# Kernel optimization log

Hardware: AMD Instinct MI355X
Metric: run time of the kernel (lower is better)

Reference implementation:

```python
import jax, jax.numpy as jnp
import numpy as np

DIM = 64  # matches init kwarg `dim`


def setup_inputs() -> dict:
    key = jax.random.key(0)
    k1, k2, k3, k4 = jax.random.split(key, 4)
    B, S, D = 16, 4096, DIM
    query = jax.random.normal(k1, (B, S, D), dtype=jnp.float32)
    key_t = jax.random.normal(k2, (B, S, D), dtype=jnp.float32)
    value = jax.random.normal(k3, (B, S, D), dtype=jnp.float32)
    mask = jax.random.randint(k4, (B, S), 0, 2).astype(jnp.bool_)
    return {"query": query, "key": key_t, "value": value, "mask": mask}


def reference(query, key, value, mask):
    # score: [B, Sq, Sk]
    scale = 1.0 / np.sqrt(DIM).astype(np.float32)
    score = jnp.einsum("bqd,bkd->bqk", query, key) * scale
    # mask reshaped to [B, 1, Sk]; True positions filled with -inf
    score = jnp.where(mask[:, None, :], -jnp.inf, score)
    attn = jax.nn.softmax(score, axis=-1)
    # dropout_p = 0.0 -> identity
    context = jnp.einsum("bqk,bkd->bqd", attn, value)
    return (context, attn)
```

## Files before the change

kernel.cpp:

```cpp
#include <hip/hip_runtime.h>
#include <hip/hip_bf16.h>
#include <cstdint>
#include <cstddef>

#define B_   16
#define S_   4096
#define D_   64
#define TQ   64
#define TK   64
#define KSTR 72
#define VSTR 72
#define PSTR 72
#define CTX_ELEMS (B_*S_*D_)

typedef __attribute__((ext_vector_type(8))) short short8;
typedef __attribute__((ext_vector_type(4))) float f32x4;

static __device__ __forceinline__ unsigned short f2bf(float f) {
  union { float f; unsigned int u; } v; v.f = f;
  unsigned int r = (v.u + 0x7FFFu + ((v.u >> 16) & 1u)) >> 16;
  return (unsigned short)r;
}

__global__ __launch_bounds__(256) void conv_bf16_kernel(
    const float* __restrict__ src, unsigned short* __restrict__ dst) {
  int i = blockIdx.x * 256 + threadIdx.x;
  const float4* s = (const float4*)src;
  float4 a = s[(size_t)i*2], b = s[(size_t)i*2 + 1];
  unsigned int u0 = (unsigned)f2bf(a.x) | ((unsigned)f2bf(a.y) << 16);
  unsigned int u1 = (unsigned)f2bf(a.z) | ((unsigned)f2bf(a.w) << 16);
  unsigned int u2 = (unsigned)f2bf(b.x) | ((unsigned)f2bf(b.y) << 16);
  unsigned int u3 = (unsigned)f2bf(b.z) | ((unsigned)f2bf(b.w) << 16);
  uint4 o; o.x = u0; o.y = u1; o.z = u2; o.w = u3;
  *(uint4*)(dst + (size_t)i * 8) = o;
}

__global__ __launch_bounds__(256) void convVt_kernel(
    const float* __restrict__ V, unsigned short* __restrict__ Vt) {
  __shared__ unsigned short lsT[D_ * VSTR];
  const int tid = threadIdx.x;
  const int b = blockIdx.y, k0 = blockIdx.x * 64;
  const float4* src = (const float4*)(V + ((size_t)(b * S_ + k0)) * D_);
#pragma unroll
  for (int i = 0; i < 4; ++i) {
    int li = tid + 256 * i;
    int row = li >> 4, c4 = li & 15;
    float4 v = src[row * 16 + c4];
    lsT[(c4 * 4 + 0) * VSTR + row] = f2bf(v.x);
    lsT[(c4 * 4 + 1) * VSTR + row] = f2bf(v.y);
    lsT[(c4 * 4 + 2) * VSTR + row] = f2bf(v.z);
    lsT[(c4 * 4 + 3) * VSTR + row] = f2bf(v.w);
  }
  __syncthreads();
#pragma unroll
  for (int i = 0; i < 2; ++i) {
    int li = tid + 256 * i;
    int d = li >> 3, c = li & 7;
    uint4 v = *(const uint4*)&lsT[d * VSTR + c * 8];
    *(uint4*)(Vt + ((size_t)(b * D_ + d)) * S_ + k0 + c * 8) = v;
  }
}

template<bool PRE>
__global__ __launch_bounds__(256, 2) void attn_kernel(
    const float* __restrict__ Q,
    const unsigned short* __restrict__ K16,
    const unsigned short* __restrict__ Vt16,
    const float* __restrict__ K32,
    const float* __restrict__ V32,
    const int* __restrict__ mask,
    float* __restrict__ out) {
  __shared__ unsigned short lsK[TK * KSTR];
  __shared__ unsigned short lsV[D_ * VSTR];
  __shared__ unsigned short lsP[4 * 16 * PSTR];
  __shared__ float lsBias[S_];

  const int tid = threadIdx.x;
  const int wave = tid >> 6, lane = tid & 63;
  const int quad = lane >> 4, n = lane & 15;

  const int g = blockIdx.x;
  const int b = (g & 7) * 2 + ((g >> 3) & 1);
  const int qt = g >> 4;
  const int qbase = qt * TQ;
  const int bS = b * S_;

  for (int i = tid; i < S_; i += 256)
    lsBias[i] = mask[bS + i] ? -1e30f : 0.0f;

  const float QSC = 0.125f * 1.44269504088896340736f;
  const int qrowA = qbase + wave * 16 + n;
  const float* qp = Q + ((size_t)(bS + qrowA)) * D_ + quad * 8;
  short8 aq0, aq1;
  {
    float4 f0 = *(const float4*)(qp);
    float4 f1 = *(const float4*)(qp + 4);
    float4 f2 = *(const float4*)(qp + 32);
    float4 f3 = *(const float4*)(qp + 36);
    aq0[0] = (short)f2bf(f0.x * QSC); aq0[1] = (short)f2bf(f0.y * QSC);
    aq0[2] = (short)f2bf(f0.z * QSC); aq0[3] = (short)f2bf(f0.w * QSC);
    aq0[4] = (short)f2bf(f1.x * QSC); aq0[5] = (short)f2bf(f1.y * QSC);
    aq0[6] = (short)f2bf(f1.z * QSC); aq0[7] = (short)f2bf(f1.w * QSC);
    aq1[0] = (short)f2bf(f2.x * QSC); aq1[1] = (short)f2bf(f2.y * QSC);
    aq1[2] = (short)f2bf(f2.z * QSC); aq1[3] = (short)f2bf(f2.w * QSC);
    aq1[4] = (short)f2bf(f3.x * QSC); aq1[5] = (short)f2bf(f3.y * QSC);
    aq1[6] = (short)f2bf(f3.z * QSC); aq1[7] = (short)f2bf(f3.w * QSC);
  }

  float l0 = 0.f, l1 = 0.f, l2 = 0.f, l3 = 0.f;
  for (int kt = 0; kt < S_ / TK; ++kt) {
    const int k0 = kt * TK;
    __syncthreads();
    if (PRE) {
#pragma unroll
      for (int i = 0; i < 2; ++i) {
        int li = tid + 256 * i;
        int row = li >> 3, c = li & 7;
        uint4 v = *(const uint4*)(K16 + ((size_t)(bS + k0 + row)) * D_ + c * 8);
        *(uint4*)&lsK[row * KSTR + c * 8] = v;
      }
    } else {
#pragma unroll
      for (int i = 0; i < 4; ++i) {
        int li = tid + 256 * i;
        int row = li >> 4, c4 = li & 15;
        float4 v = *(const float4*)(K32 + ((size_t)(bS + k0 + row)) * D_ + c4 * 4);
        unsigned int u0 = (unsigned)f2bf(v.x) | ((unsigned)f2bf(v.y) << 16);
        unsigned int u1 = (unsigned)f2bf(v.z) | ((unsigned)f2bf(v.w) << 16);
        uint2 uu; uu.x = u0; uu.y = u1;
        *(uint2*)&lsK[row * KSTR + c4 * 4] = uu;
      }
    }
    __syncthreads();
#pragma unroll
    for (int ch = 0; ch < 4; ++ch) {
      short8 kb0 = *(const short8*)&lsK[(ch * 16 + n) * KSTR + quad * 8];
      short8 kb1 = *(const short8*)&lsK[(ch * 16 + n) * KSTR + 32 + quad * 8];
      f32x4 c = {0.f, 0.f, 0.f, 0.f};
      c = __builtin_amdgcn_mfma_f32_16x16x32_bf16(aq0, kb0, c, 0, 0, 0);
      c = __builtin_amdgcn_mfma_f32_16x16x32_bf16(aq1, kb1, c, 0, 0, 0);
      float bias = lsBias[k0 + ch * 16 + n];
      l0 += exp2f(c[0] + bias);
      l1 += exp2f(c[1] + bias);
      l2 += exp2f(c[2] + bias);
      l3 += exp2f(c[3] + bias);
    }
  }
  float rl[4];
  {
    float t[4] = {l0, l1, l2, l3};
#pragma unroll
    for (int r = 0; r < 4; ++r) {
      float x = t[r];
      x += __shfl_xor(x, 1); x += __shfl_xor(x, 2);
      x += __shfl_xor(x, 4); x += __shfl_xor(x, 8);
      rl[r] = 1.0f / x;
    }
  }

  f32x4 oc0 = {0.f,0.f,0.f,0.f}, oc1 = {0.f,0.f,0.f,0.f};
  f32x4 oc2 = {0.f,0.f,0.f,0.f}, oc3 = {0.f,0.f,0.f,0.f};
  float* attn = out + CTX_ELEMS;
  for (int kt = 0; kt < S_ / TK; ++kt) {
    const int k0 = kt * TK;
    __syncthreads();
    if (PRE) {
#pragma unroll
      for (int i = 0; i < 2; ++i) {
        int li = tid + 256 * i;
        int row = li >> 3, c = li & 7;
        uint4 v = *(const uint4*)(K16 + ((size_t)(bS + k0 + row)) * D_ + c * 8);
        *(uint4*)&lsK[row * KSTR + c * 8] = v;
      }
#pragma unroll
      for (int i = 0; i < 2; ++i) {
        int li = tid + 256 * i;
        int d = li >> 3, c = li & 7;
        uint4 v = *(const uint4*)(Vt16 + ((size_t)(b * D_ + d)) * S_ + k0 + c * 8);
        *(uint4*)&lsV[d * VSTR + c * 8] = v;
      }
    } else {
#pragma unroll
      for (int i = 0; i < 4; ++i) {
        int li = tid + 256 * i;
        int row = li >> 4, c4 = li & 15;
        float4 v = *(const float4*)(K32 + ((size_t)(bS + k0 + row)) * D_ + c4 * 4);
        unsigned int u0 = (unsigned)f2bf(v.x) | ((unsigned)f2bf(v.y) << 16);
        unsigned int u1 = (unsigned)f2bf(v.z) | ((unsigned)f2bf(v.w) << 16);
        uint2 uu; uu.x = u0; uu.y = u1;
        *(uint2*)&lsK[row * KSTR + c4 * 4] = uu;
        float4 vv = *(const float4*)(V32 + ((size_t)(bS + k0 + row)) * D_ + c4 * 4);
        lsV[(c4 * 4 + 0) * VSTR + row] = f2bf(vv.x);
        lsV[(c4 * 4 + 1) * VSTR + row] = f2bf(vv.y);
        lsV[(c4 * 4 + 2) * VSTR + row] = f2bf(vv.z);
        lsV[(c4 * 4 + 3) * VSTR + row] = f2bf(vv.w);
      }
    }
    __syncthreads();
#pragma unroll
    for (int ch = 0; ch < 4; ++ch) {
      short8 kb0 = *(const short8*)&lsK[(ch * 16 + n) * KSTR + quad * 8];
      short8 kb1 = *(const short8*)&lsK[(ch * 16 + n) * KSTR + 32 + quad * 8];
      f32x4 c = {0.f, 0.f, 0.f, 0.f};
      c = __builtin_amdgcn_mfma_f32_16x16x32_bf16(aq0, kb0, c, 0, 0, 0);
      c = __builtin_amdgcn_mfma_f32_16x16x32_bf16(aq1, kb1, c, 0, 0, 0);
      float bias = lsBias[k0 + ch * 16 + n];
#pragma unroll
      for (int r = 0; r < 4; ++r) {
        float p = exp2f(c[r] + bias) * rl[r];
        int qr = qbase + wave * 16 + quad * 4 + r;
        __builtin_nontemporal_store(
            p, attn + ((size_t)(bS + qr)) * S_ + k0 + ch * 16 + n);
        lsP[(wave * 16 + quad * 4 + r) * PSTR + ch * 16 + n] = f2bf(p);
      }
    }
#pragma unroll
    for (int ks = 0; ks < 2; ++ks) {
      short8 ap = *(const short8*)&lsP[(wave * 16 + n) * PSTR + ks * 32 + quad * 8];
      short8 bv0 = *(const short8*)&lsV[(0 * 16 + n) * VSTR + ks * 32 + quad * 8];
      short8 bv1 = *(const short8*)&lsV[(1 * 16 + n) * VSTR + ks * 32 + quad * 8];
      short8 bv2 = *(const short8*)&lsV[(2 * 16 + n) * VSTR + ks * 32 + quad * 8];
      short8 bv3 = *(const short8*)&lsV[(3 * 16 + n) * VSTR + ks * 32 + quad * 8];
      oc0 = __builtin_amdgcn_mfma_f32_16x16x32_bf16(ap, bv0, oc0, 0, 0, 0);
      oc1 = __builtin_amdgcn_mfma_f32_16x16x32_bf16(ap, bv1, oc1, 0, 0, 0);
      oc2 = __builtin_amdgcn_mfma_f32_16x16x32_bf16(ap, bv2, oc2, 0, 0, 0);
      oc3 = __builtin_amdgcn_mfma_f32_16x16x32_bf16(ap, bv3, oc3, 0, 0, 0);
    }
  }
#pragma unroll
  for (int r = 0; r < 4; ++r) {
    int qr = qbase + wave * 16 + quad * 4 + r;
    float* op = out + ((size_t)(bS + qr)) * D_ + n;
    __builtin_nontemporal_store(oc0[r], op + 0);
    __builtin_nontemporal_store(oc1[r], op + 16);
    __builtin_nontemporal_store(oc2[r], op + 32);
    __builtin_nontemporal_store(oc3[r], op + 48);
  }
}

extern "C" void kernel_launch(void* const* d_in, const int* in_sizes, int n_in,
                              void* d_out, int out_size, void* d_ws, size_t ws_size,
                              hipStream_t stream) {
  const float* q = (const float*)d_in[0];
  const float* k = (const float*)d_in[1];
  const float* v = (const float*)d_in[2];
  const int* mask = (const int*)d_in[3];
  float* out = (float*)d_out;

  const size_t elems = (size_t)B_ * S_ * D_;
  const size_t need = 2 * elems * sizeof(unsigned short);
  if (ws_size >= need) {
    unsigned short* K16 = (unsigned short*)d_ws;
    unsigned short* Vt16 = K16 + elems;
    conv_bf16_kernel<<<(int)(elems / 8 / 256), 256, 0, stream>>>(k, K16);
    convVt_kernel<<<dim3(S_ / 64, B_), 256, 0, stream>>>(v, Vt16);
    attn_kernel<true><<<B_ * (S_ / TQ), 256, 0, stream>>>(
        q, K16, Vt16, k, v, mask, out);
  } else {
    attn_kernel<false><<<B_ * (S_ / TQ), 256, 0, stream>>>(
        q, nullptr, nullptr, k, v, mask, out);
  }
}
```

Before: 1.257 ms.

## Prefetch K/V tiles into registers, transpose QK MFMA, vectorize attn stores

Register-prefetches the next K (and Vt) tile during the current tile's compute, replacing the synchronous global-to-LDS loads, and uses lighter raw barriers with an explicit lgkmcnt wait. Swaps the MFMA operand order so each lane holds four consecutive key columns of one query row, which allows 16-byte vectorized nontemporal attention stores, packed bf16 P writes and a float4 bias read. The mask-to-bias fill is also vectorized and occupancy is raised to 3 blocks per SM. The prefetch registers may raise register pressure against the new launch bound.

```diff
diff --git a/kernel.cpp b/kernel.cpp
--- a/kernel.cpp
+++ b/kernel.cpp
@@ -8,6 +8,7 @@
 #define D_   64
 #define TQ   64
 #define TK   64
+#define NT   (S_ / TK)
 #define KSTR 72
 #define VSTR 72
 #define PSTR 72
@@ -61,8 +62,20 @@
   }
 }
 
+#define BAR_PLAIN() do { if constexpr (PRE) { \
+    asm volatile("" ::: "memory"); \
+    __builtin_amdgcn_s_barrier(); \
+    asm volatile("" ::: "memory"); \
+  } else { __syncthreads(); } } while (0)
+
+#define BAR_LGKM() do { if constexpr (PRE) { \
+    asm volatile("s_waitcnt lgkmcnt(0)" ::: "memory"); \
+    __builtin_amdgcn_s_barrier(); \
+    asm volatile("" ::: "memory"); \
+  } else { __syncthreads(); } } while (0)
+
 template<bool PRE>
-__global__ __launch_bounds__(256, 2) void attn_kernel(
+__global__ __launch_bounds__(256, 3) void attn_kernel(
     const float* __restrict__ Q,
     const unsigned short* __restrict__ K16,
     const unsigned short* __restrict__ Vt16,
@@ -73,7 +86,7 @@
   __shared__ unsigned short lsK[TK * KSTR];
   __shared__ unsigned short lsV[D_ * VSTR];
   __shared__ unsigned short lsP[4 * 16 * PSTR];
-  __shared__ float lsBias[S_];
+  __shared__ __align__(16) float lsBias[S_];
 
   const int tid = threadIdx.x;
   const int wave = tid >> 6, lane = tid & 63;
@@ -85,12 +98,23 @@
   const int qbase = qt * TQ;
   const int bS = b * S_;
 
-  for (int i = tid; i < S_; i += 256)
-    lsBias[i] = mask[bS + i] ? -1e30f : 0.0f;
+  {
+    const uint4* mi = (const uint4*)(mask + bS);
+    float4* bo = (float4*)lsBias;
+    for (int i = tid; i < S_ / 4; i += 256) {
+      uint4 m = mi[i];
+      float4 f;
+      f.x = m.x ? -1e30f : 0.0f;
+      f.y = m.y ? -1e30f : 0.0f;
+      f.z = m.z ? -1e30f : 0.0f;
+      f.w = m.w ? -1e30f : 0.0f;
+      bo[i] = f;
+    }
+  }
 
   const float QSC = 0.125f * 1.44269504088896340736f;
-  const int qrowA = qbase + wave * 16 + n;
-  const float* qp = Q + ((size_t)(bS + qrowA)) * D_ + quad * 8;
+  const int qrow = qbase + wave * 16 + n;
+  const float* qp = Q + ((size_t)(bS + qrow)) * D_ + quad * 8;
   short8 aq0, aq1;
   {
     float4 f0 = *(const float4*)(qp);
@@ -107,17 +131,24 @@
     aq1[6] = (short)f2bf(f3.z * QSC); aq1[7] = (short)f2bf(f3.w * QSC);
   }
 
+  const int r0 = tid >> 3, c0 = tid & 7;
+
+  uint4 sk0, sk1, sv0, sv1;
+
   float l0 = 0.f, l1 = 0.f, l2 = 0.f, l3 = 0.f;
-  for (int kt = 0; kt < S_ / TK; ++kt) {
+  if constexpr (PRE) {
+    sk0 = *(const uint4*)(K16 + ((size_t)(bS + r0)) * D_ + c0 * 8);
+    sk1 = *(const uint4*)(K16 + ((size_t)(bS + r0 + 32)) * D_ + c0 * 8);
+  }
+  for (int kt = 0; kt < NT; ++kt) {
     const int k0 = kt * TK;
-    __syncthreads();
-    if (PRE) {
-#pragma unroll
-      for (int i = 0; i < 2; ++i) {
-        int li = tid + 256 * i;
-        int row = li >> 3, c = li & 7;
-        uint4 v = *(const uint4*)(K16 + ((size_t)(bS + k0 + row)) * D_ + c * 8);
-        *(uint4*)&lsK[row * KSTR + c * 8] = v;
+    BAR_PLAIN();
+    if constexpr (PRE) {
+      *(uint4*)&lsK[r0 * KSTR + c0 * 8] = sk0;
+      *(uint4*)&lsK[(r0 + 32) * KSTR + c0 * 8] = sk1;
+      if (kt + 1 < NT) {
+        sk0 = *(const uint4*)(K16 + ((size_t)(bS + k0 + TK + r0)) * D_ + c0 * 8);
+        sk1 = *(const uint4*)(K16 + ((size_t)(bS + k0 + TK + r0 + 32)) * D_ + c0 * 8);
       }
     } else {
 #pragma unroll
@@ -131,53 +162,48 @@
         *(uint2*)&lsK[row * KSTR + c4 * 4] = uu;
       }
     }
-    __syncthreads();
+    BAR_LGKM();
 #pragma unroll
     for (int ch = 0; ch < 4; ++ch) {
       short8 kb0 = *(const short8*)&lsK[(ch * 16 + n) * KSTR + quad * 8];
       short8 kb1 = *(const short8*)&lsK[(ch * 16 + n) * KSTR + 32 + quad * 8];
       f32x4 c = {0.f, 0.f, 0.f, 0.f};
-      c = __builtin_amdgcn_mfma_f32_16x16x32_bf16(aq0, kb0, c, 0, 0, 0);
-      c = __builtin_amdgcn_mfma_f32_16x16x32_bf16(aq1, kb1, c, 0, 0, 0);
-      float bias = lsBias[k0 + ch * 16 + n];
-      l0 += exp2f(c[0] + bias);
-      l1 += exp2f(c[1] + bias);
-      l2 += exp2f(c[2] + bias);
-      l3 += exp2f(c[3] + bias);
-    }
-  }
-  float rl[4];
-  {
-    float t[4] = {l0, l1, l2, l3};
-#pragma unroll
-    for (int r = 0; r < 4; ++r) {
-      float x = t[r];
-      x += __shfl_xor(x, 1); x += __shfl_xor(x, 2);
-      x += __shfl_xor(x, 4); x += __shfl_xor(x, 8);
-      rl[r] = 1.0f / x;
-    }
-  }
+      c = __builtin_amdgcn_mfma_f32_16x16x32_bf16(kb0, aq0, c, 0, 0, 0);
+      c = __builtin_amdgcn_mfma_f32_16x16x32_bf16(kb1, aq1, c, 0, 0, 0);
+      const float4 bb = *(const float4*)&lsBias[k0 + ch * 16 + quad * 4];
+      l0 += exp2f(c[0] + bb.x);
+      l1 += exp2f(c[1] + bb.y);
+      l2 += exp2f(c[2] + bb.z);
+      l3 += exp2f(c[3] + bb.w);
+    }
+  }
+  if constexpr (PRE) {
+    sk0 = *(const uint4*)(K16 + ((size_t)(bS + r0)) * D_ + c0 * 8);
+    sk1 = *(const uint4*)(K16 + ((size_t)(bS + r0 + 32)) * D_ + c0 * 8);
+    sv0 = *(const uint4*)(Vt16 + ((size_t)(b * D_ + r0)) * S_ + c0 * 8);
+    sv1 = *(const uint4*)(Vt16 + ((size_t)(b * D_ + r0 + 32)) * S_ + c0 * 8);
+  }
+  float lt = (l0 + l1) + (l2 + l3);
+  lt += __shfl_xor(lt, 16);
+  lt += __shfl_xor(lt, 32);
+  const float rl = 1.0f / lt;
 
   f32x4 oc0 = {0.f,0.f,0.f,0.f}, oc1 = {0.f,0.f,0.f,0.f};
   f32x4 oc2 = {0.f,0.f,0.f,0.f}, oc3 = {0.f,0.f,0.f,0.f};
-  float* attn = out + CTX_ELEMS;
-  for (int kt = 0; kt < S_ / TK; ++kt) {
+  float* attnRow = out + CTX_ELEMS + ((size_t)(bS + qrow)) * S_;
+  for (int kt = 0; kt < NT; ++kt) {
     const int k0 = kt * TK;
-    __syncthreads();
-    if (PRE) {
-#pragma unroll
-      for (int i = 0; i < 2; ++i) {
-        int li = tid + 256 * i;
-        int row = li >> 3, c = li & 7;
-        uint4 v = *(const uint4*)(K16 + ((size_t)(bS + k0 + row)) * D_ + c * 8);
-        *(uint4*)&lsK[row * KSTR + c * 8] = v;
-      }
-#pragma unroll
-      for (int i = 0; i < 2; ++i) {
-        int li = tid + 256 * i;
-        int d = li >> 3, c = li & 7;
-        uint4 v = *(const uint4*)(Vt16 + ((size_t)(b * D_ + d)) * S_ + k0 + c * 8);
-        *(uint4*)&lsV[d * VSTR + c * 8] = v;
+    BAR_PLAIN();
+    if constexpr (PRE) {
+      *(uint4*)&lsK[r0 * KSTR + c0 * 8] = sk0;
+      *(uint4*)&lsK[(r0 + 32) * KSTR + c0 * 8] = sk1;
+      *(uint4*)&lsV[r0 * VSTR + c0 * 8] = sv0;
+      *(uint4*)&lsV[(r0 + 32) * VSTR + c0 * 8] = sv1;
+      if (kt + 1 < NT) {
+        sk0 = *(const uint4*)(K16 + ((size_t)(bS + k0 + TK + r0)) * D_ + c0 * 8);
+        sk1 = *(const uint4*)(K16 + ((size_t)(bS + k0 + TK + r0 + 32)) * D_ + c0 * 8);
+        sv0 = *(const uint4*)(Vt16 + ((size_t)(b * D_ + r0)) * S_ + k0 + TK + c0 * 8);
+        sv1 = *(const uint4*)(Vt16 + ((size_t)(b * D_ + r0 + 32)) * S_ + k0 + TK + c0 * 8);
       }
     } else {
 #pragma unroll
@@ -196,23 +222,25 @@
         lsV[(c4 * 4 + 3) * VSTR + row] = f2bf(vv.w);
       }
     }
-    __syncthreads();
+    BAR_LGKM();
 #pragma unroll
     for (int ch = 0; ch < 4; ++ch) {
       short8 kb0 = *(const short8*)&lsK[(ch * 16 + n) * KSTR + quad * 8];
       short8 kb1 = *(const short8*)&lsK[(ch * 16 + n) * KSTR + 32 + quad * 8];
       f32x4 c = {0.f, 0.f, 0.f, 0.f};
-      c = __builtin_amdgcn_mfma_f32_16x16x32_bf16(aq0, kb0, c, 0, 0, 0);
-      c = __builtin_amdgcn_mfma_f32_16x16x32_bf16(aq1, kb1, c, 0, 0, 0);
-      float bias = lsBias[k0 + ch * 16 + n];
-#pragma unroll
-      for (int r = 0; r < 4; ++r) {
-        float p = exp2f(c[r] + bias) * rl[r];
-        int qr = qbase + wave * 16 + quad * 4 + r;
-        __builtin_nontemporal_store(
-            p, attn + ((size_t)(bS + qr)) * S_ + k0 + ch * 16 + n);
-        lsP[(wave * 16 + quad * 4 + r) * PSTR + ch * 16 + n] = f2bf(p);
-      }
+      c = __builtin_amdgcn_mfma_f32_16x16x32_bf16(kb0, aq0, c, 0, 0, 0);
+      c = __builtin_amdgcn_mfma_f32_16x16x32_bf16(kb1, aq1, c, 0, 0, 0);
+      const float4 bb = *(const float4*)&lsBias[k0 + ch * 16 + quad * 4];
+      f32x4 p;
+      p[0] = exp2f(c[0] + bb.x) * rl;
+      p[1] = exp2f(c[1] + bb.y) * rl;
+      p[2] = exp2f(c[2] + bb.z) * rl;
+      p[3] = exp2f(c[3] + bb.w) * rl;
+      __builtin_nontemporal_store(p, (f32x4*)(attnRow + k0 + ch * 16 + quad * 4));
+      uint2 pw;
+      pw.x = (unsigned)f2bf(p[0]) | ((unsigned)f2bf(p[1]) << 16);
+      pw.y = (unsigned)f2bf(p[2]) | ((unsigned)f2bf(p[3]) << 16);
+      *(uint2*)&lsP[(wave * 16 + n) * PSTR + ch * 16 + quad * 4] = pw;
     }
 #pragma unroll
     for (int ks = 0; ks < 2; ++ks) {
```

Result: slower. 1.289 ms (+2.6%).
